# Kernel tuning notes

Measured on AMD Instinct MI355X. Metric: run time of the kernel, lower is better.

The kernel has to match this reference:

```python
import jax, jax.numpy as jnp
import numpy as np

# Llama-2-7B-like config with GQA
T, D, N, K, H = 2048, 4096, 32, 8, 128
THETA = 10000.0


def _rope(x, positions):
    """Split-ordering RoPE on last dim H of x: [..., T, heads, H]."""
    half = H // 2
    inv_freq = 1.0 / (THETA ** (jnp.arange(half, dtype=jnp.float32) / half))  # theta^(-2i/H)
    ang = positions.astype(jnp.float32)[:, None] * inv_freq[None, :]          # [T, half]
    cos = jnp.cos(ang)[:, None, :]
    sin = jnp.sin(ang)[:, None, :]
    x1, x2 = x[..., :half], x[..., half:]
    return jnp.concatenate([x1 * cos - x2 * sin, x2 * cos + x1 * sin], axis=-1).astype(x.dtype)


def setup_inputs() -> dict:
    key = jax.random.key(0)
    ks = jax.random.split(key, 5)
    s_in = 1.0 / np.sqrt(D)
    s_out = 1.0 / np.sqrt(N * H)
    return {
        "x": jax.random.normal(ks[0], (T, D), jnp.float32),
        "positions": jnp.arange(T, dtype=jnp.int32),
        "w_q": jax.random.normal(ks[1], (D, N, H), jnp.float32) * s_in,
        "w_k": jax.random.normal(ks[2], (D, K, H), jnp.float32) * s_in,
        "w_v": jax.random.normal(ks[3], (D, K, H), jnp.float32) * s_in,
        "w_o": jax.random.normal(ks[4], (N, H, D), jnp.float32) * s_out,
    }


def reference(x, positions, w_q, w_k, w_v, w_o):
    """Prefill path: fused QKV proj + RoPE + causal GQA attention + o_proj."""
    G = N // K  # query heads per kv head
    q = jnp.einsum('td,dnh->tnh', x, w_q)
    k = jnp.einsum('sd,dkh->skh', x, w_k)
    v = jnp.einsum('sd,dkh->skh', x, w_v)
    q = _rope(q, positions)
    k = _rope(k, positions)
    qg = q.reshape(T, K, G, H)
    scores = jnp.einsum('tkgh,skh->kgts', qg, k) * (H ** -0.5)
    causal = positions[:, None] >= positions[None, :]  # [T, S]
    scores = jnp.where(causal[None, None], scores, jnp.finfo(scores.dtype).min)
    probs = jax.nn.softmax(scores, axis=-1)
    out = jnp.einsum('kgts,skh->tkgh', probs, v).reshape(T, N, H)
    return jnp.einsum('tnh,nhd->td', out, w_o)
```

## Files before the change

### kernel.cpp

```cpp
#include <hip/hip_runtime.h>
#include <hip/hip_bf16.h>
#include <math.h>

#define T_SEQ   2048
#define D_MODEL 4096
#define N_Q     32
#define N_KV    8
#define HDIM    128
#define NH      (N_Q * HDIM)
#define KH      (N_KV * HDIM)
#define QKV_W   (NH + 2 * KH)

using bf16   = __hip_bfloat16;
using short8 = __attribute__((ext_vector_type(8))) short;
using floatx4 = __attribute__((ext_vector_type(4))) float;

__device__ __forceinline__ void load_lds16(const bf16* g, bf16* l) {
  __builtin_amdgcn_global_load_lds((const __attribute__((address_space(1))) void*)g,
                                   (__attribute__((address_space(3))) void*)l,
                                   16, 0, 0);
}
__device__ __forceinline__ void store_out(bf16* p, float v) { *p = __float2bfloat16(v); }
__device__ __forceinline__ void store_out(float* p, float v) { *p = v; }

__global__ void cvt_bf16_kernel(const float* __restrict__ src, bf16* __restrict__ dst, int n4) {
  int i = blockIdx.x * 256 + threadIdx.x;
  if (i < n4) {
    const float4 v = ((const float4*)src)[i];
    union { bf16 h[4]; unsigned long long u; } o;
    o.h[0] = __float2bfloat16(v.x); o.h[1] = __float2bfloat16(v.y);
    o.h[2] = __float2bfloat16(v.z); o.h[3] = __float2bfloat16(v.w);
    ((unsigned long long*)dst)[i] = o.u;
  }
}

__global__ void transpose_cvt(const float* __restrict__ src, bf16* __restrict__ dst,
                              int R, int C) {
  __shared__ float tile[32][33];
  const int bx = blockIdx.x * 32;
  const int by = blockIdx.y * 32;
  const int tx = threadIdx.x & 31, ty = threadIdx.x >> 5;
#pragma unroll
  for (int i = 0; i < 32; i += 8)
    tile[ty + i][tx] = src[(size_t)(by + ty + i) * C + bx + tx];
  __syncthreads();
#pragma unroll
  for (int i = 0; i < 32; i += 8)
    dst[(size_t)(bx + ty + i) * R + by + tx] = __float2bfloat16(tile[tx][ty + i]);
}

__global__ void transpose_bf16(const bf16* __restrict__ src, bf16* __restrict__ dst,
                               int R, int C, int src_stride) {
  __shared__ bf16 tile[32][33];
  const int bx = blockIdx.x * 32;
  const int by = blockIdx.y * 32;
  const int tx = threadIdx.x & 31, ty = threadIdx.x >> 5;
#pragma unroll
  for (int i = 0; i < 32; i += 8)
    tile[ty + i][tx] = src[(size_t)(by + ty + i) * src_stride + bx + tx];
  __syncthreads();
#pragma unroll
  for (int i = 0; i < 32; i += 8)
    dst[(size_t)(bx + ty + i) * R + by + tx] = tile[tx][ty + i];
}

template <typename OutT>
__global__ __launch_bounds__(256)
void gemm_bt(const bf16* __restrict__ A, const bf16* __restrict__ B,
             OutT* __restrict__ C, int M, int N, int Kc) {
  __shared__ bf16 As[128 * 32];
  __shared__ bf16 Bs[128 * 32];
  const int tid  = threadIdx.x;
  const int lane = tid & 63;
  const int wave = tid >> 6;
  const int bm = blockIdx.x * 128;
  const int bn = blockIdx.y * 128;
  const int wm = (wave >> 1) * 64;
  const int wn = (wave & 1) * 64;
  const int r = lane & 15, q = lane >> 4;

  floatx4 acc[4][4];
  const floatx4 zero = {0.f, 0.f, 0.f, 0.f};
#pragma unroll
  for (int i = 0; i < 4; i++)
#pragma unroll
    for (int j = 0; j < 4; j++) acc[i][j] = zero;

  const int srow = wave * 32 + (lane >> 2);
  const int scol = (lane & 3) * 8;
  const bf16* gA = A + (size_t)(bm + srow) * Kc + scol;
  const bf16* gB = B + (size_t)(bn + srow) * Kc + scol;
  bf16* lA = As + wave * 32 * 32;
  bf16* lB = Bs + wave * 32 * 32;

  for (int k0 = 0; k0 < Kc; k0 += 32) {
    __syncthreads();
    load_lds16(gA + k0,                   lA);
    load_lds16(gA + k0 + 16 * (size_t)Kc, lA + 16 * 32);
    load_lds16(gB + k0,                   lB);
    load_lds16(gB + k0 + 16 * (size_t)Kc, lB + 16 * 32);
    __syncthreads();

    short8 af[4], bfr[4];
#pragma unroll
    for (int mt = 0; mt < 4; mt++)
      af[mt] = *(const short8*)(As + (wm + mt * 16 + r) * 32 + q * 8);
#pragma unroll
    for (int nt = 0; nt < 4; nt++)
      bfr[nt] = *(const short8*)(Bs + (wn + nt * 16 + r) * 32 + q * 8);
#pragma unroll
    for (int mt = 0; mt < 4; mt++)
#pragma unroll
      for (int nt = 0; nt < 4; nt++)
        acc[mt][nt] = __builtin_amdgcn_mfma_f32_16x16x32_bf16(af[mt], bfr[nt], acc[mt][nt], 0, 0, 0);
  }

#pragma unroll
  for (int mt = 0; mt < 4; mt++)
#pragma unroll
    for (int nt = 0; nt < 4; nt++)
#pragma unroll
      for (int reg = 0; reg < 4; reg++) {
        const int row = bm + wm + mt * 16 + q * 4 + reg;
        const int col = bn + wn + nt * 16 + r;
        store_out(&C[(size_t)row * N + col], acc[mt][nt][reg]);
      }
}

__global__ void rope_kernel(const bf16* __restrict__ QKV, const int* __restrict__ positions,
                            bf16* __restrict__ Q, bf16* __restrict__ Kr) {
  const int t = blockIdx.x;
  const float pos = (float)positions[t];
  const int hh = threadIdx.x & 63;
  const float inv = exp2f(-(float)hh * 0.2076205092954967f);
  float sn, cs; sincosf(pos * inv, &sn, &cs);
  const float SCL = 0.12751744868673310f;
  const bf16* row = QKV + (size_t)t * QKV_W;
  for (int idx = threadIdx.x; idx < N_Q * 64; idx += 256) {
    const int n = idx >> 6;
    const float x1 = __bfloat162float(row[n * HDIM + hh]);
    const float x2 = __bfloat162float(row[n * HDIM + hh + 64]);
    Q[(size_t)t * NH + n * HDIM + hh]      = __float2bfloat16((x1 * cs - x2 * sn) * SCL);
    Q[(size_t)t * NH + n * HDIM + hh + 64] = __float2bfloat16((x2 * cs + x1 * sn) * SCL);
  }
  for (int idx = threadIdx.x; idx < N_KV * 64; idx += 256) {
    const int kh = idx >> 6;
    const float x1 = __bfloat162float(row[NH + kh * HDIM + hh]);
    const float x2 = __bfloat162float(row[NH + kh * HDIM + hh + 64]);
    Kr[(size_t)t * KH + kh * HDIM + hh]      = __float2bfloat16(x1 * cs - x2 * sn);
    Kr[(size_t)t * KH + kh * HDIM + hh + 64] = __float2bfloat16(x2 * cs + x1 * sn);
  }
}

__global__ __launch_bounds__(256, 2)
void flash_attn(const bf16* __restrict__ Q, const bf16* __restrict__ Kk,
                const bf16* __restrict__ Vt, bf16* __restrict__ O) {
  const int id = blockIdx.x;
  const int n  = id & 31;
  const int kh = n >> 2;
  const int bt = (id < 256) ? (15 - (id >> 5)) : ((id - 256) >> 5);
  const int t0 = bt * 128;
  const int tid = threadIdx.x, lane = tid & 63, w = tid >> 6;
  const int r = lane & 15, q = lane >> 4;

  __shared__ bf16 Ks[64][128];
  __shared__ bf16 Vs[128][64];
  __shared__ bf16 Ps[4][32][72];

  short8 qf[2][4];
#pragma unroll
  for (int mf = 0; mf < 2; mf++) {
    const bf16* qrow = Q + (size_t)(t0 + w * 32 + mf * 16 + r) * NH + n * HDIM;
#pragma unroll
    for (int ks = 0; ks < 4; ks++)
      qf[mf][ks] = *(const short8*)(qrow + ks * 32 + q * 8);
  }

  floatx4 o_acc[2][8];
  const floatx4 zero = {0.f, 0.f, 0.f, 0.f};
#pragma unroll
  for (int mf = 0; mf < 2; mf++)
#pragma unroll
    for (int i = 0; i < 8; i++) o_acc[mf][i] = zero;
  float m_i[2][4], l_i[2][4];
#pragma unroll
  for (int mf = 0; mf < 2; mf++)
#pragma unroll
    for (int i = 0; i < 4; i++) { m_i[mf][i] = -INFINITY; l_i[mf][i] = 0.f; }

  const int nIter = 2 * bt + 2;
  for (int it = 0; it < nIter; ++it) {
    const int s0 = it * 64;
    __syncthreads();
#pragma unroll
    for (int c = 0; c < 4; c++) {
      const int chunk = tid + 256 * c;
      const int s = chunk >> 4, cx = chunk & 15;
      *(short8*)(&Ks[s][(cx ^ (s & 7)) * 8]) =
          *(const short8*)(Kk + (size_t)(s0 + s) * KH + kh * HDIM + cx * 8);
    }
#pragma unroll
    for (int c = 0; c < 4; c++) {
      const int chunk = tid + 256 * c;
      const int h = chunk >> 3, sc = chunk & 7;
      *(short8*)(&Vs[h][(sc ^ (h & 7)) * 8]) =
          *(const short8*)(Vt + ((size_t)kh * HDIM + h) * T_SEQ + s0 + sc * 8);
    }
    __syncthreads();

    floatx4 sa[2][4];
#pragma unroll
    for (int mf = 0; mf < 2; mf++)
#pragma unroll
      for (int nt = 0; nt < 4; nt++) sa[mf][nt] = zero;
#pragma unroll
    for (int ks = 0; ks < 4; ks++)
#pragma unroll
      for (int nt = 0; nt < 4; nt++) {
        const int krow = nt * 16 + r;
        const short8 kb = *(const short8*)(&Ks[krow][(((ks * 4 + q) ^ (krow & 7))) * 8]);
#pragma unroll
        for (int mf = 0; mf < 2; mf++)
          sa[mf][nt] = __builtin_amdgcn_mfma_f32_16x16x32_bf16(qf[mf][ks], kb, sa[mf][nt], 0, 0, 0);
      }

#pragma unroll
    for (int mf = 0; mf < 2; mf++) {
      const int rbase = t0 + w * 32 + mf * 16;
      if (s0 + 63 > rbase) {
#pragma unroll
        for (int nt = 0; nt < 4; nt++)
#pragma unroll
          for (int reg = 0; reg < 4; reg++) {
            const int trow = rbase + q * 4 + reg;
            const int scol = s0 + nt * 16 + r;
            if (scol > trow) sa[mf][nt][reg] = -INFINITY;
          }
      }
      float mloc[4];
#pragma unroll
      for (int reg = 0; reg < 4; reg++) {
        float v = fmaxf(fmaxf(sa[mf][0][reg], sa[mf][1][reg]),
                        fmaxf(sa[mf][2][reg], sa[mf][3][reg]));
        v = fmaxf(v, __shfl_xor(v, 1));
        v = fmaxf(v, __shfl_xor(v, 2));
        v = fmaxf(v, __shfl_xor(v, 4));
        v = fmaxf(v, __shfl_xor(v, 8));
        mloc[reg] = v;
      }
      float alpha[4], lloc[4];
#pragma unroll
      for (int reg = 0; reg < 4; reg++) {
        const float mnew = fmaxf(m_i[mf][reg], mloc[reg]);
        alpha[reg] = exp2f(m_i[mf][reg] - mnew);
        m_i[mf][reg] = mnew;
        lloc[reg] = 0.f;
      }
#pragma unroll
      for (int nt = 0; nt < 4; nt++)
#pragma unroll
        for (int reg = 0; reg < 4; reg++) {
          const float p = exp2f(sa[mf][nt][reg] - m_i[mf][reg]);
          lloc[reg] += p;
          Ps[w][mf * 16 + q * 4 + reg][nt * 16 + r] = __float2bfloat16(p);
        }
#pragma unroll
      for (int reg = 0; reg < 4; reg++) {
        float v = lloc[reg];
        v += __shfl_xor(v, 1); v += __shfl_xor(v, 2);
        v += __shfl_xor(v, 4); v += __shfl_xor(v, 8);
        l_i[mf][reg] = l_i[mf][reg] * alpha[reg] + v;
      }
#pragma unroll
      for (int ht = 0; ht < 8; ht++)
#pragma unroll
        for (int reg = 0; reg < 4; reg++)
          o_acc[mf][ht][reg] *= alpha[reg];
    }

    __asm__ volatile("s_waitcnt lgkmcnt(0)" ::: "memory");

#pragma unroll
    for (int ks = 0; ks < 2; ks++) {
      short8 pa[2];
#pragma unroll
      for (int mf = 0; mf < 2; mf++)
        pa[mf] = *(const short8*)(&Ps[w][mf * 16 + r][ks * 32 + q * 8]);
#pragma unroll
      for (int ht = 0; ht < 8; ht++) {
        const int vrow = ht * 16 + r;
        const short8 vb = *(const short8*)(&Vs[vrow][(((ks * 4 + q) ^ (vrow & 7))) * 8]);
#pragma unroll
        for (int mf = 0; mf < 2; mf++)
          o_acc[mf][ht] = __builtin_amdgcn_mfma_f32_16x16x32_bf16(pa[mf], vb, o_acc[mf][ht], 0, 0, 0);
      }
    }
  }

#pragma unroll
  for (int mf = 0; mf < 2; mf++)
#pragma unroll
    for (int reg = 0; reg < 4; reg++) {
      const float inv_l = 1.0f / l_i[mf][reg];
      const int trow = t0 + w * 32 + mf * 16 + q * 4 + reg;
#pragma unroll
      for (int ht = 0; ht < 8; ht++)
        O[(size_t)trow * NH + n * HDIM + ht * 16 + r] =
            __float2bfloat16(o_acc[mf][ht][reg] * inv_l);
    }
}

extern "C" void kernel_launch(void* const* d_in, const int* in_sizes, int n_in,
                              void* d_out, int out_size, void* d_ws, size_t ws_size,
                              hipStream_t stream) {
  (void)in_sizes; (void)n_in; (void)out_size; (void)ws_size;
  const float* x   = (const float*)d_in[0];
  const int* pos   = (const int*)d_in[1];
  const float* w_q = (const float*)d_in[2];
  const float* w_k = (const float*)d_in[3];
  const float* w_v = (const float*)d_in[4];
  const float* w_o = (const float*)d_in[5];
  float* out = (float*)d_out;

  char* ws = (char*)d_ws;
  bf16* xb   = (bf16*)(ws);
  bf16* Bq   = (bf16*)(ws + 16777216ULL);
  bf16* QKV  = (bf16*)(ws + 67108864ULL);
  bf16* Qr   = (bf16*)(ws + 92274688ULL);
  bf16* Kr   = (bf16*)(ws + 109051904ULL);
  bf16* Vt   = (bf16*)(ws + 113246208ULL);
  bf16* Oatt = (bf16*)(ws + 117440512ULL);
  bf16* woT  = Bq;

  cvt_bf16_kernel<<<(T_SEQ * D_MODEL / 4 + 255) / 256, 256, 0, stream>>>(x, xb, T_SEQ * D_MODEL / 4);
  transpose_cvt<<<dim3(NH / 32, D_MODEL / 32), 256, 0, stream>>>(w_q, Bq, D_MODEL, NH);
  transpose_cvt<<<dim3(KH / 32, D_MODEL / 32), 256, 0, stream>>>(w_k, Bq + (size_t)NH * D_MODEL, D_MODEL, KH);
  transpose_cvt<<<dim3(KH / 32, D_MODEL / 32), 256, 0, stream>>>(w_v, Bq + (size_t)(NH + KH) * D_MODEL, D_MODEL, KH);
  gemm_bt<bf16><<<dim3(T_SEQ / 128, QKV_W / 128), 256, 0, stream>>>(xb, Bq, QKV, T_SEQ, QKV_W, D_MODEL);
  rope_kernel<<<T_SEQ, 256, 0, stream>>>(QKV, pos, Qr, Kr);
  transpose_bf16<<<dim3(KH / 32, T_SEQ / 32), 256, 0, stream>>>(QKV + NH + KH, Vt, T_SEQ, KH, QKV_W);
  transpose_cvt<<<dim3(D_MODEL / 32, NH / 32), 256, 0, stream>>>(w_o, woT, NH, D_MODEL);
  flash_attn<<<dim3(512), 256, 0, stream>>>(Qr, Kr, Vt, Oatt);
  gemm_bt<float><<<dim3(T_SEQ / 128, D_MODEL / 128), 256, 0, stream>>>(Oatt, woT, out, T_SEQ, D_MODEL, NH);
}
```

Baseline: 567.9 us.

## Fuse RoPE and V transpose into QKV GEMM epilogue; widen K-tile with swizzled LDS

The QKV projection GEMM now applies RoPE (with the Q scale) in its epilogue and writes transposed V directly. A bf16 tile staged in shared memory makes this possible, so the intermediate QKV buffer, the separate rope kernel and the V transpose kernel are gone. The GEMM main loop moves from a 32-wide to a 64-wide K step with XOR-swizzled LDS layout to reduce bank conflicts and halve barrier count. Weight transposes use 64x64 tiles with float4 loads and 16-byte stores. The epilogue recomputes sincos per element and uses scalar stores, which could add ALU cost.

```diff
diff --git a/kernel.cpp b/kernel.cpp
--- a/kernel.cpp
+++ b/kernel.cpp
@@ -20,8 +20,6 @@
                                    (__attribute__((address_space(3))) void*)l,
                                    16, 0, 0);
 }
-__device__ __forceinline__ void store_out(bf16* p, float v) { *p = __float2bfloat16(v); }
-__device__ __forceinline__ void store_out(float* p, float v) { *p = v; }
 
 __global__ void cvt_bf16_kernel(const float* __restrict__ src, bf16* __restrict__ dst, int n4) {
   int i = blockIdx.x * 256 + threadIdx.x;
@@ -34,42 +32,46 @@
   }
 }
 
-__global__ void transpose_cvt(const float* __restrict__ src, bf16* __restrict__ dst,
-                              int R, int C) {
-  __shared__ float tile[32][33];
-  const int bx = blockIdx.x * 32;
-  const int by = blockIdx.y * 32;
-  const int tx = threadIdx.x & 31, ty = threadIdx.x >> 5;
-#pragma unroll
-  for (int i = 0; i < 32; i += 8)
-    tile[ty + i][tx] = src[(size_t)(by + ty + i) * C + bx + tx];
+__global__ __launch_bounds__(256)
+void transpose_cvt(const float* __restrict__ src, bf16* __restrict__ dst, int R, int C) {
+  __shared__ float tile[64][65];
+  const int bx = blockIdx.x * 64;
+  const int by = blockIdx.y * 64;
+  const int c4 = (threadIdx.x & 15) * 4;
+  const int r0 = threadIdx.x >> 4;
+#pragma unroll
+  for (int i = 0; i < 4; i++) {
+    const float4 v = *(const float4*)&src[(size_t)(by + r0 + i * 16) * C + bx + c4];
+    tile[r0 + i * 16][c4 + 0] = v.x;
+    tile[r0 + i * 16][c4 + 1] = v.y;
+    tile[r0 + i * 16][c4 + 2] = v.z;
+    tile[r0 + i * 16][c4 + 3] = v.w;
+  }
   __syncthreads();
-#pragma unroll
-  for (int i = 0; i < 32; i += 8)
-    dst[(size_t)(bx + ty + i) * R + by + tx] = __float2bfloat16(tile[tx][ty + i]);
-}
-
-__global__ void transpose_bf16(const bf16* __restrict__ src, bf16* __restrict__ dst,
-                               int R, int C, int src_stride) {
-  __shared__ bf16 tile[32][33];
-  const int bx = blockIdx.x * 32;
-  const int by = blockIdx.y * 32;
-  const int tx = threadIdx.x & 31, ty = threadIdx.x >> 5;
-#pragma unroll
-  for (int i = 0; i < 32; i += 8)
-    tile[ty + i][tx] = src[(size_t)(by + ty + i) * src_stride + bx + tx];
-  __syncthreads();
-#pragma unroll
-  for (int i = 0; i < 32; i += 8)
-    dst[(size_t)(bx + ty + i) * R + by + tx] = tile[tx][ty + i];
-}
-
-template <typename OutT>
+  const int cc = threadIdx.x >> 2;
+  const int rq = (threadIdx.x & 3) * 16;
+  union { bf16 h[8]; short8 s; } o0, o1;
+#pragma unroll
+  for (int j = 0; j < 8; j++) {
+    o0.h[j] = __float2bfloat16(tile[rq + j][cc]);
+    o1.h[j] = __float2bfloat16(tile[rq + 8 + j][cc]);
+  }
+  bf16* d = dst + (size_t)(bx + cc) * R + by + rq;
+  *(short8*)(d)     = o0.s;
+  *(short8*)(d + 8) = o1.s;
+}
+
+#define CS_STRIDE 137
+template <int EPI>
 __global__ __launch_bounds__(256)
-void gemm_bt(const bf16* __restrict__ A, const bf16* __restrict__ B,
-             OutT* __restrict__ C, int M, int N, int Kc) {
-  __shared__ bf16 As[128 * 32];
-  __shared__ bf16 Bs[128 * 32];
+void gemm_bt2(const bf16* __restrict__ A, const bf16* __restrict__ B,
+              float* __restrict__ Cf, int N, int Kc,
+              const int* __restrict__ positions,
+              bf16* __restrict__ Qo, bf16* __restrict__ Ko, bf16* __restrict__ Vo) {
+  __shared__ bf16 smem[(EPI == 2) ? (128 * CS_STRIDE) : (128 * 128)];
+  bf16* As = smem;
+  bf16* Bs = smem + 128 * 64;
+
   const int tid  = threadIdx.x;
   const int lane = tid & 63;
   const int wave = tid >> 6;
@@ -86,69 +88,93 @@
 #pragma unroll
     for (int j = 0; j < 4; j++) acc[i][j] = zero;
 
-  const int srow = wave * 32 + (lane >> 2);
-  const int scol = (lane & 3) * 8;
-  const bf16* gA = A + (size_t)(bm + srow) * Kc + scol;
-  const bf16* gB = B + (size_t)(bn + srow) * Kc + scol;
-  bf16* lA = As + wave * 32 * 32;
-  bf16* lB = Bs + wave * 32 * 32;
-
-  for (int k0 = 0; k0 < Kc; k0 += 32) {
-    __syncthreads();
-    load_lds16(gA + k0,                   lA);
-    load_lds16(gA + k0 + 16 * (size_t)Kc, lA + 16 * 32);
-    load_lds16(gB + k0,                   lB);
-    load_lds16(gB + k0 + 16 * (size_t)Kc, lB + 16 * 32);
-    __syncthreads();
-
-    short8 af[4], bfr[4];
+  const int rl = lane >> 3, ch = lane & 7;
+  const int srow = wave * 32 + rl;
+  const int gch = ch ^ rl;
+  const bf16* gA = A + (size_t)(bm + srow) * Kc + gch * 8;
+  const bf16* gB = B + (size_t)(bn + srow) * Kc + gch * 8;
+
+  for (int k0 = 0; k0 < Kc; k0 += 64) {
+    __syncthreads();
+#pragma unroll
+    for (int i = 0; i < 4; i++)
+      load_lds16(gA + k0 + (size_t)i * 8 * Kc, As + (wave * 32 + i * 8) * 64);
+#pragma unroll
+    for (int i = 0; i < 4; i++)
+      load_lds16(gB + k0 + (size_t)i * 8 * Kc, Bs + (wave * 32 + i * 8) * 64);
+    __syncthreads();
+
+#pragma unroll
+    for (int ks = 0; ks < 2; ks++) {
+      short8 af[4], bfr[4];
+#pragma unroll
+      for (int mt = 0; mt < 4; mt++)
+        af[mt] = *(const short8*)(As + (wm + mt * 16 + r) * 64 + ((ks * 4 + q) ^ (r & 7)) * 8);
+#pragma unroll
+      for (int nt = 0; nt < 4; nt++)
+        bfr[nt] = *(const short8*)(Bs + (wn + nt * 16 + r) * 64 + ((ks * 4 + q) ^ (r & 7)) * 8);
+#pragma unroll
+      for (int mt = 0; mt < 4; mt++)
+#pragma unroll
+        for (int nt = 0; nt < 4; nt++)
+          acc[mt][nt] = __builtin_amdgcn_mfma_f32_16x16x32_bf16(af[mt], bfr[nt], acc[mt][nt], 0, 0, 0);
+    }
+  }
+
+  if (EPI == 1) {
 #pragma unroll
     for (int mt = 0; mt < 4; mt++)
-      af[mt] = *(const short8*)(As + (wm + mt * 16 + r) * 32 + q * 8);
-#pragma unroll
-    for (int nt = 0; nt < 4; nt++)
-      bfr[nt] = *(const short8*)(Bs + (wn + nt * 16 + r) * 32 + q * 8);
+#pragma unroll
+      for (int nt = 0; nt < 4; nt++)
+#pragma unroll
+        for (int reg = 0; reg < 4; reg++) {
+          const int row = bm + wm + mt * 16 + q * 4 + reg;
+          const int col = bn + wn + nt * 16 + r;
+          Cf[(size_t)row * N + col] = acc[mt][nt][reg];
+        }
+  } else {
+    __syncthreads();
 #pragma unroll
     for (int mt = 0; mt < 4; mt++)
 #pragma unroll
       for (int nt = 0; nt < 4; nt++)
-        acc[mt][nt] = __builtin_amdgcn_mfma_f32_16x16x32_bf16(af[mt], bfr[nt], acc[mt][nt], 0, 0, 0);
-  }
-
-#pragma unroll
-  for (int mt = 0; mt < 4; mt++)
-#pragma unroll
-    for (int nt = 0; nt < 4; nt++)
-#pragma unroll
-      for (int reg = 0; reg < 4; reg++) {
-        const int row = bm + wm + mt * 16 + q * 4 + reg;
-        const int col = bn + wn + nt * 16 + r;
-        store_out(&C[(size_t)row * N + col], acc[mt][nt][reg]);
-      }
-}
-
-__global__ void rope_kernel(const bf16* __restrict__ QKV, const int* __restrict__ positions,
-                            bf16* __restrict__ Q, bf16* __restrict__ Kr) {
-  const int t = blockIdx.x;
-  const float pos = (float)positions[t];
-  const int hh = threadIdx.x & 63;
-  const float inv = exp2f(-(float)hh * 0.2076205092954967f);
-  float sn, cs; sincosf(pos * inv, &sn, &cs);
-  const float SCL = 0.12751744868673310f;
-  const bf16* row = QKV + (size_t)t * QKV_W;
-  for (int idx = threadIdx.x; idx < N_Q * 64; idx += 256) {
-    const int n = idx >> 6;
-    const float x1 = __bfloat162float(row[n * HDIM + hh]);
-    const float x2 = __bfloat162float(row[n * HDIM + hh + 64]);
-    Q[(size_t)t * NH + n * HDIM + hh]      = __float2bfloat16((x1 * cs - x2 * sn) * SCL);
-    Q[(size_t)t * NH + n * HDIM + hh + 64] = __float2bfloat16((x2 * cs + x1 * sn) * SCL);
-  }
-  for (int idx = threadIdx.x; idx < N_KV * 64; idx += 256) {
-    const int kh = idx >> 6;
-    const float x1 = __bfloat162float(row[NH + kh * HDIM + hh]);
-    const float x2 = __bfloat162float(row[NH + kh * HDIM + hh + 64]);
-    Kr[(size_t)t * KH + kh * HDIM + hh]      = __float2bfloat16(x1 * cs - x2 * sn);
-    Kr[(size_t)t * KH + kh * HDIM + hh + 64] = __float2bfloat16(x2 * cs + x1 * sn);
+#pragma unroll
+        for (int reg = 0; reg < 4; reg++)
+          smem[(wm + mt * 16 + q * 4 + reg) * CS_STRIDE + wn + nt * 16 + r] =
+              __float2bfloat16(acc[mt][nt][reg]);
+    __syncthreads();
+
+    const int hn = blockIdx.y;
+    if (hn < N_Q + N_KV) {
+      const float SCL = 0.12751744868673310f;
+      const bool isQ = (hn < N_Q);
+      bf16* base = isQ ? (Qo + (size_t)bm * NH + hn * HDIM)
+                       : (Ko + (size_t)bm * KH + (hn - N_Q) * HDIM);
+      const int ostride = isQ ? NH : KH;
+      for (int idx = tid; idx < 128 * 64; idx += 256) {
+        const int row = idx >> 6, h = idx & 63;
+        const float x1 = __bfloat162float(smem[row * CS_STRIDE + h]);
+        const float x2 = __bfloat162float(smem[row * CS_STRIDE + h + 64]);
+        const float pos = (float)positions[bm + row];
+        const float inv = exp2f(-(float)h * 0.20762050593046013f);
+        float sn, cs; sincosf(pos * inv, &sn, &cs);
+        float o1 = x1 * cs - x2 * sn;
+        float o2 = x2 * cs + x1 * sn;
+        if (isQ) { o1 *= SCL; o2 *= SCL; }
+        bf16* d = base + (size_t)row * ostride;
+        d[h]      = __float2bfloat16(o1);
+        d[h + 64] = __float2bfloat16(o2);
+      }
+    } else {
+      const int kh = hn - (N_Q + N_KV);
+      for (int idx = tid; idx < 128 * 32; idx += 256) {
+        const int h = idx >> 5, r4 = (idx & 31) * 4;
+        union { bf16 h4[4]; unsigned long long u; } o;
+#pragma unroll
+        for (int j = 0; j < 4; j++) o.h4[j] = smem[(r4 + j) * CS_STRIDE + h];
+        *(unsigned long long*)(Vo + ((size_t)kh * HDIM + h) * T_SEQ + bm + r4) = o.u;
+      }
+    }
   }
 }
 
@@ -324,22 +350,25 @@
 
   char* ws = (char*)d_ws;
   bf16* xb   = (bf16*)(ws);
-  bf16* Bq   = (bf16*)(ws + 16777216ULL);
-  bf16* QKV  = (bf16*)(ws + 67108864ULL);
-  bf16* Qr   = (bf16*)(ws + 92274688ULL);
-  bf16* Kr   = (bf16*)(ws + 109051904ULL);
-  bf16* Vt   = (bf16*)(ws + 113246208ULL);
-  bf16* Oatt = (bf16*)(ws + 117440512ULL);
+  bf16* Bq   = (bf16*)(ws + (16ULL << 20));
+  bf16* Qr   = (bf16*)(ws + (64ULL << 20));
+  bf16* Kr   = (bf16*)(ws + (80ULL << 20));
+  bf16* Vt   = (bf16*)(ws + (84ULL << 20));
+  bf16* Oatt = (bf16*)(ws + (88ULL << 20));
   bf16* woT  = Bq;
 
   cvt_bf16_kernel<<<(T_SEQ * D_MODEL / 4 + 255) / 256, 256, 0, stream>>>(x, xb, T_SEQ * D_MODEL / 4);
-  transpose_cvt<<<dim3(NH / 32, D_MODEL / 32), 256, 0, stream>>>(w_q, Bq, D_MODEL, NH);
-  transpose_cvt<<<dim3(KH / 32, D_MODEL / 32), 256, 0, stream>>>(w_k, Bq + (size_t)NH * D_MODEL, D_MODEL, KH);
-  transpose_cvt<<<dim3(KH / 32, D_MODEL / 32), 256, 0, stream>>>(w_v, Bq + (size_t)(NH + KH) * D_MODEL, D_MODEL, KH);
-  gemm_bt<bf16><<<dim3(T_SEQ / 128, QKV_W / 128), 256, 0, stream>>>(xb, Bq, QKV, T_SEQ, QKV_W, D_MODEL);
-  rope_kernel<<<T_SEQ, 256, 0, stream>>>(QKV, pos, Qr, Kr);
-  transpose_bf16<<<dim3(KH / 32, T_SEQ / 32), 256, 0, stream>>>(QKV + NH + KH, Vt, T_SEQ, KH, QKV_W);
-  transpose_cvt<<<dim3(D_MODEL / 32, NH / 32), 256, 0, stream>>>(w_o, woT, NH, D_MODEL);
+  transpose_cvt<<<dim3(NH / 64, D_MODEL / 64), 256, 0, stream>>>(w_q, Bq, D_MODEL, NH);
+  transpose_cvt<<<dim3(KH / 64, D_MODEL / 64), 256, 0, stream>>>(w_k, Bq + (size_t)NH * D_MODEL, D_MODEL, KH);
+  transpose_cvt<<<dim3(KH / 64, D_MODEL / 64), 256, 0, stream>>>(w_v, Bq + (size_t)(NH + KH) * D_MODEL, D_MODEL, KH);
+
+  gemm_bt2<2><<<dim3(T_SEQ / 128, QKV_W / 128), 256, 0, stream>>>(
+      xb, Bq, nullptr, QKV_W, D_MODEL, pos, Qr, Kr, Vt);
+
+  transpose_cvt<<<dim3(D_MODEL / 64, NH / 64), 256, 0, stream>>>(w_o, woT, NH, D_MODEL);
+
   flash_attn<<<dim3(512), 256, 0, stream>>>(Qr, Kr, Vt, Oatt);
-  gemm_bt<float><<<dim3(T_SEQ / 128, D_MODEL / 128), 256, 0, stream>>>(Oatt, woT, out, T_SEQ, D_MODEL, NH);
-}
+
+  gemm_bt2<1><<<dim3(T_SEQ / 128, D_MODEL / 128), 256, 0, stream>>>(
+      Oatt, woT, out, D_MODEL, NH, nullptr, nullptr, nullptr, nullptr);
+}
```

After: 533.9 us. -6.0%, faster.
